# Kernel optimization log

Hardware: AMD Instinct MI355X
Metric: run time of the kernel (lower is better)

Reference implementation:

```python
import jax, jax.numpy as jnp
import numpy as np


def setup_inputs() -> dict:
    key = jax.random.key(0)
    k1, k2 = jax.random.split(key)
    H = W = 4096
    input1 = jax.random.normal(k1, (1, 1, H, W), dtype=jnp.float32)   # moving image
    input2 = jax.random.normal(k2, (1, 2, H, W), dtype=jnp.float32)   # dense flow (dH, dW)
    return {"input1": input1, "input2": input2}


def reference(input1, input2):
    # input1: [B=1, C=1, H, W] image; input2: [B=1, 2, H, W] displacement field
    B, C, H, W = input1.shape
    f32 = jnp.float32

    # identity mesh (matches torch.linspace outer-product construction)
    h_mesh = jnp.broadcast_to(jnp.arange(H, dtype=f32)[None, :, None], (B, H, W))
    w_mesh = jnp.broadcast_to(jnp.arange(W, dtype=f32)[None, None, :], (B, H, W))

    # warped sampling coordinates, shifted by +1 for the zero-padding border
    H_up = (input2[:, 0] + h_mesh).reshape(-1) + 1.0   # [B*H*W]
    W_up = (input2[:, 1] + w_mesh).reshape(-1) + 1.0

    # zero-pad image by 1 pixel on each spatial side
    img = jnp.pad(input1, ((0, 0), (0, 0), (1, 1), (1, 1)))  # [B, C, H+2, W+2]
    Hp, Wp = H + 2, W + 2

    hf = jnp.floor(H_up).astype(jnp.int32)
    hc = hf + 1
    wf = jnp.floor(W_up).astype(jnp.int32)
    wc = wf + 1
    hf = jnp.clip(hf, 0, Hp - 1)
    hc = jnp.clip(hc, 0, Hp - 1)
    wf = jnp.clip(wf, 0, Wp - 1)
    wc = jnp.clip(wc, 0, Wp - 1)

    img_flat = img.reshape(-1)  # B = C = 1
    val_000 = img_flat[hf * Wp + wf]
    val_010 = img_flat[hc * Wp + wf]
    val_001 = img_flat[hf * Wp + wc]
    val_011 = img_flat[hc * Wp + wc]

    dH = hc.astype(f32) - H_up
    dW = wc.astype(f32) - W_up
    out = (val_000 * (dW * dH)
           + val_010 * (dW * (1.0 - dH))
           + val_001 * ((1.0 - dW) * dH)
           + val_011 * ((1.0 - dW) * (1.0 - dH)))

    # [B*H*W] -> [B, H, W, C] -> [B, C, H, W]
    return out.reshape(B, H, W, C).transpose(0, 3, 1, 2)
```

## Files before the change

kernel.cpp:

```cpp
#include <hip/hip_runtime.h>


#define IMG_H 4096
#define IMG_W 4096

typedef float f2  __attribute__((ext_vector_type(2)));
typedef float f2u __attribute__((ext_vector_type(2), aligned(4)));

__global__ __launch_bounds__(256) void warp_bilinear_kernel(
    const float* __restrict__ img,
    const float* __restrict__ flow,
    float* __restrict__ out)
{
    const int HW   = IMG_H * IMG_W;
    const int lane = threadIdx.x & 63;
    const int wv   = threadIdx.x >> 6;
    const int w0   = blockIdx.x * 128 + lane * 2;
    const int h0   = blockIdx.y * 8 + wv * 2;

    int rowidx[2];
    rowidx[0] = h0 * IMG_W + w0;
    rowidx[1] = rowidx[0] + IMG_W;

    f2 fh[2], fw[2];
    #pragma unroll
    for (int r = 0; r < 2; ++r)
        fh[r] = __builtin_nontemporal_load((const f2*)(flow + rowidx[r]));
    #pragma unroll
    for (int r = 0; r < 2; ++r)
        fw[r] = __builtin_nontemporal_load((const f2*)(flow + HW + rowidx[r]));

    int   o0[2][2], o1[2][2];
    float a0x[2][2], a0y[2][2], a1x[2][2], a1y[2][2];

    #pragma unroll
    for (int r = 0; r < 2; ++r) {
        #pragma unroll
        for (int c = 0; c < 2; ++c) {
            const int h = h0 + r;
            const int w = w0 + c;
            float Hu = (fh[r][c] + (float)h) + 1.0f;
            float Wu = (fw[r][c] + (float)w) + 1.0f;

            int hf = (int)floorf(Hu);
            int wf = (int)floorf(Wu);
            int hc = hf + 1;
            int wc = wf + 1;

            int hfc = min(max(hf, 0), IMG_H + 1);
            int hcc = min(max(hc, 0), IMG_H + 1);
            int wfc = min(max(wf, 0), IMG_W + 1);
            int wcc = min(max(wc, 0), IMG_W + 1);

            float dH = (float)hcc - Hu;
            float dW = (float)wcc - Wu;

            int rf = hfc - 1, rc = hcc - 1, cf = wfc - 1, cc = wcc - 1;
            bool rf_in = (unsigned)rf < IMG_H;
            bool rc_in = (unsigned)rc < IMG_H;
            bool cf_in = (unsigned)cf < IMG_W;
            bool cc_in = (unsigned)cc < IMG_W;

            int rf_cl = min(max(rf, 0), IMG_H - 1);
            int rc_cl = min(max(rc, 0), IMG_H - 1);
            int cf_cl = min(max(cf, 0), IMG_W - 1);
            int cc_cl = min(max(cc, 0), IMG_W - 1);
            int cb    = min(max(cf, 0), IMG_W - 2);

            int sf = cf_cl - cb;
            int sc = cc_cl - cb;

            o0[r][c] = (rf_cl << 12) + cb;
            o1[r][c] = (rc_cl << 12) + cb;

            float A = dW * dH;
            float B = dW * (1.0f - dH);
            float C = (1.0f - dW) * dH;
            float D = (1.0f - dW) * (1.0f - dH);
            float w00 = (rf_in && cf_in) ? A : 0.0f;
            float w10 = (rc_in && cf_in) ? B : 0.0f;
            float w01 = (rf_in && cc_in) ? C : 0.0f;
            float w11 = (rc_in && cc_in) ? D : 0.0f;

            a0x[r][c] = (sf ? 0.0f : w00) + (sc ? 0.0f : w01);
            a0y[r][c] = (sf ? w00 : 0.0f) + (sc ? w01 : 0.0f);
            a1x[r][c] = (sf ? 0.0f : w10) + (sc ? 0.0f : w11);
            a1y[r][c] = (sf ? w10 : 0.0f) + (sc ? w11 : 0.0f);
        }
    }

    f2u p0[2][2], p1[2][2];
    #pragma unroll
    for (int r = 0; r < 2; ++r) {
        #pragma unroll
        for (int c = 0; c < 2; ++c) {
            p0[r][c] = *(const f2u*)(img + o0[r][c]);
            p1[r][c] = *(const f2u*)(img + o1[r][c]);
        }
    }

    #pragma unroll
    for (int r = 0; r < 2; ++r) {
        f2 res;
        #pragma unroll
        for (int c = 0; c < 2; ++c) {
            res[c] = p0[r][c].x * a0x[r][c] + p0[r][c].y * a0y[r][c]
                   + p1[r][c].x * a1x[r][c] + p1[r][c].y * a1y[r][c];
        }
        __builtin_nontemporal_store(res, (f2*)(out + rowidx[r]));
    }
}

extern "C" void kernel_launch(void* const* d_in, const int* in_sizes, int n_in,
                              void* d_out, int out_size, void* d_ws, size_t ws_size,
                              hipStream_t stream) {
    const float* img  = (const float*)d_in[0];
    const float* flow = (const float*)d_in[1];
    float* out = (float*)d_out;

    dim3 grid(IMG_W / 128, IMG_H / 8);
    dim3 block(256);
    warp_bilinear_kernel<<<grid, block, 0, stream>>>(img, flow, out);
}
```

Baseline: 243.6 us.

## Stage image tile with halo in shared memory for bilinear gathers

Each block now cooperatively loads a 16x128 image tile plus an 8-pixel halo into LDS using vectorized loads. The bilinear taps are read from shared memory instead of global memory, with a fallback to global loads whenever a tap falls outside the staged window. The block tile also grows so each thread handles four rows instead of two. The goal is to replace scattered global gathers with cheap LDS reads, at the cost of extra halo traffic, a block-wide barrier and more LDS use per block.

```diff
diff --git a/kernel.cpp b/kernel.cpp
--- a/kernel.cpp
+++ b/kernel.cpp
@@ -3,111 +3,165 @@
 
 #define IMG_H 4096
 #define IMG_W 4096
+#define TR 16
+#define TC 128
+#define HALO 8
+#define SR (TR + 2 * HALO)
+#define SC (TC + 2 * HALO)
+#define SC4 (SC / 4)
+#define NCHUNK (SR * SC4)
 
 typedef float f2  __attribute__((ext_vector_type(2)));
 typedef float f2u __attribute__((ext_vector_type(2), aligned(4)));
+typedef float f4  __attribute__((ext_vector_type(4)));
 
 __global__ __launch_bounds__(256) void warp_bilinear_kernel(
     const float* __restrict__ img,
     const float* __restrict__ flow,
     float* __restrict__ out)
 {
+    __shared__ float tile[SR * SC];
+
     const int HW   = IMG_H * IMG_W;
-    const int lane = threadIdx.x & 63;
-    const int wv   = threadIdx.x >> 6;
-    const int w0   = blockIdx.x * 128 + lane * 2;
-    const int h0   = blockIdx.y * 8 + wv * 2;
-
-    int rowidx[2];
-    rowidx[0] = h0 * IMG_W + w0;
-    rowidx[1] = rowidx[0] + IMG_W;
-
-    f2 fh[2], fw[2];
-    #pragma unroll
-    for (int r = 0; r < 2; ++r)
-        fh[r] = __builtin_nontemporal_load((const f2*)(flow + rowidx[r]));
-    #pragma unroll
-    for (int r = 0; r < 2; ++r)
-        fw[r] = __builtin_nontemporal_load((const f2*)(flow + HW + rowidx[r]));
-
-    int   o0[2][2], o1[2][2];
-    float a0x[2][2], a0y[2][2], a1x[2][2], a1y[2][2];
+    const int tid  = threadIdx.x;
+    const int lane = tid & 63;
+    const int wv   = tid >> 6;
+    const int w0   = blockIdx.x * TC + lane * 2;
+    const int h0   = blockIdx.y * TR + wv * 4;
+    const int r_lo = blockIdx.y * TR - HALO;
+    const int c_lo = blockIdx.x * TC - HALO;
 
     #pragma unroll
-    for (int r = 0; r < 2; ++r) {
-        #pragma unroll
-        for (int c = 0; c < 2; ++c) {
-            const int h = h0 + r;
-            const int w = w0 + c;
-            float Hu = (fh[r][c] + (float)h) + 1.0f;
-            float Wu = (fw[r][c] + (float)w) + 1.0f;
-
-            int hf = (int)floorf(Hu);
-            int wf = (int)floorf(Wu);
-            int hc = hf + 1;
-            int wc = wf + 1;
-
-            int hfc = min(max(hf, 0), IMG_H + 1);
-            int hcc = min(max(hc, 0), IMG_H + 1);
-            int wfc = min(max(wf, 0), IMG_W + 1);
-            int wcc = min(max(wc, 0), IMG_W + 1);
-
-            float dH = (float)hcc - Hu;
-            float dW = (float)wcc - Wu;
-
-            int rf = hfc - 1, rc = hcc - 1, cf = wfc - 1, cc = wcc - 1;
-            bool rf_in = (unsigned)rf < IMG_H;
-            bool rc_in = (unsigned)rc < IMG_H;
-            bool cf_in = (unsigned)cf < IMG_W;
-            bool cc_in = (unsigned)cc < IMG_W;
-
-            int rf_cl = min(max(rf, 0), IMG_H - 1);
-            int rc_cl = min(max(rc, 0), IMG_H - 1);
-            int cf_cl = min(max(cf, 0), IMG_W - 1);
-            int cc_cl = min(max(cc, 0), IMG_W - 1);
-            int cb    = min(max(cf, 0), IMG_W - 2);
-
-            int sf = cf_cl - cb;
-            int sc = cc_cl - cb;
-
-            o0[r][c] = (rf_cl << 12) + cb;
-            o1[r][c] = (rc_cl << 12) + cb;
-
-            float A = dW * dH;
-            float B = dW * (1.0f - dH);
-            float C = (1.0f - dW) * dH;
-            float D = (1.0f - dW) * (1.0f - dH);
-            float w00 = (rf_in && cf_in) ? A : 0.0f;
-            float w10 = (rc_in && cf_in) ? B : 0.0f;
-            float w01 = (rf_in && cc_in) ? C : 0.0f;
-            float w11 = (rc_in && cc_in) ? D : 0.0f;
-
-            a0x[r][c] = (sf ? 0.0f : w00) + (sc ? 0.0f : w01);
-            a0y[r][c] = (sf ? w00 : 0.0f) + (sc ? w01 : 0.0f);
-            a1x[r][c] = (sf ? 0.0f : w10) + (sc ? 0.0f : w11);
-            a1y[r][c] = (sf ? w10 : 0.0f) + (sc ? w11 : 0.0f);
+    for (int it = 0; it < 5; ++it) {
+        int t = tid + it * 256;
+        if (t < NCHUNK) {
+            int i  = t / SC4;
+            int m  = t - i * SC4;
+            int gr = min(max(r_lo + i, 0), IMG_H - 1);
+            int gc = min(max(c_lo + 4 * m, 0), IMG_W - 4);
+            f4 v = *(const f4*)(img + gr * IMG_W + gc);
+            *(f4*)(tile + i * SC + 4 * m) = v;
         }
     }
 
-    f2u p0[2][2], p1[2][2];
+    int rowidx[4];
+    f2  fh[4], fw[4];
     #pragma unroll
-    for (int r = 0; r < 2; ++r) {
-        #pragma unroll
-        for (int c = 0; c < 2; ++c) {
-            p0[r][c] = *(const f2u*)(img + o0[r][c]);
-            p1[r][c] = *(const f2u*)(img + o1[r][c]);
-        }
-    }
+    for (int r = 0; r < 4; ++r)
+        rowidx[r] = (h0 + r) * IMG_W + w0;
+    #pragma unroll
+    for (int r = 0; r < 4; ++r)
+        fh[r] = __builtin_nontemporal_load((const f2*)(flow + rowidx[r]));
+    #pragma unroll
+    for (int r = 0; r < 4; ++r)
+        fw[r] = __builtin_nontemporal_load((const f2*)(flow + HW + rowidx[r]));
+
+    __syncthreads();
 
     #pragma unroll
-    for (int r = 0; r < 2; ++r) {
-        f2 res;
+    for (int g = 0; g < 2; ++g) {
+        int   li0[2][2], li1[2][2];
+        int   ob0[2][2], ob1[2][2];
+        float a0x[2][2], a0y[2][2], a1x[2][2], a1y[2][2];
+        bool  ok = true;
+
         #pragma unroll
-        for (int c = 0; c < 2; ++c) {
-            res[c] = p0[r][c].x * a0x[r][c] + p0[r][c].y * a0y[r][c]
-                   + p1[r][c].x * a1x[r][c] + p1[r][c].y * a1y[r][c];
+        for (int rr = 0; rr < 2; ++rr) {
+            const int r = 2 * g + rr;
+            #pragma unroll
+            for (int c = 0; c < 2; ++c) {
+                const int h = h0 + r;
+                const int w = w0 + c;
+                float Hu = (fh[r][c] + (float)h) + 1.0f;
+                float Wu = (fw[r][c] + (float)w) + 1.0f;
+
+                int hf = (int)floorf(Hu);
+                int wf = (int)floorf(Wu);
+                int hc = hf + 1;
+                int wc = wf + 1;
+
+                int hfc = min(max(hf, 0), IMG_H + 1);
+                int hcc = min(max(hc, 0), IMG_H + 1);
+                int wfc = min(max(wf, 0), IMG_W + 1);
+                int wcc = min(max(wc, 0), IMG_W + 1);
+
+                float dH = (float)hcc - Hu;
+                float dW = (float)wcc - Wu;
+
+                int rf = hfc - 1, rc = hcc - 1, cf = wfc - 1, cc = wcc - 1;
+                bool rf_in = (unsigned)rf < IMG_H;
+                bool rc_in = (unsigned)rc < IMG_H;
+                bool cf_in = (unsigned)cf < IMG_W;
+                bool cc_in = (unsigned)cc < IMG_W;
+
+                int rf_cl = min(max(rf, 0), IMG_H - 1);
+                int rc_cl = min(max(rc, 0), IMG_H - 1);
+                int cf_cl = min(max(cf, 0), IMG_W - 1);
+                int cc_cl = min(max(cc, 0), IMG_W - 1);
+                int cb    = min(max(cf, 0), IMG_W - 2);
+
+                int sf = cf_cl - cb;
+                int sc = cc_cl - cb;
+
+                int i0 = rf_cl - r_lo;
+                int i1 = rc_cl - r_lo;
+                int jb = cb - c_lo;
+                ok = ok && ((unsigned)i0 < SR) && ((unsigned)i1 < SR)
+                        && ((unsigned)jb < (SC - 1));
+                li0[rr][c] = i0 * SC + jb;
+                li1[rr][c] = i1 * SC + jb;
+                ob0[rr][c] = (rf_cl << 12) + cb;
+                ob1[rr][c] = (rc_cl << 12) + cb;
+
+                float A = dW * dH;
+                float B = dW * (1.0f - dH);
+                float C = (1.0f - dW) * dH;
+                float D = (1.0f - dW) * (1.0f - dH);
+                float w00 = (rf_in && cf_in) ? A : 0.0f;
+                float w10 = (rc_in && cf_in) ? B : 0.0f;
+                float w01 = (rf_in && cc_in) ? C : 0.0f;
+                float w11 = (rc_in && cc_in) ? D : 0.0f;
+
+                a0x[rr][c] = (sf ? 0.0f : w00) + (sc ? 0.0f : w01);
+                a0y[rr][c] = (sf ? w00 : 0.0f) + (sc ? w01 : 0.0f);
+                a1x[rr][c] = (sf ? 0.0f : w10) + (sc ? 0.0f : w11);
+                a1y[rr][c] = (sf ? w10 : 0.0f) + (sc ? w11 : 0.0f);
+            }
         }
-        __builtin_nontemporal_store(res, (f2*)(out + rowidx[r]));
+
+        float q0x[2][2], q0y[2][2], q1x[2][2], q1y[2][2];
+        if (__builtin_expect(ok, 1)) {
+            #pragma unroll
+            for (int rr = 0; rr < 2; ++rr)
+                #pragma unroll
+                for (int c = 0; c < 2; ++c) {
+                    q0x[rr][c] = tile[li0[rr][c]];
+                    q0y[rr][c] = tile[li0[rr][c] + 1];
+                    q1x[rr][c] = tile[li1[rr][c]];
+                    q1y[rr][c] = tile[li1[rr][c] + 1];
+                }
+        } else {
+            #pragma unroll
+            for (int rr = 0; rr < 2; ++rr)
+                #pragma unroll
+                for (int c = 0; c < 2; ++c) {
+                    f2u p0 = *(const f2u*)(img + ob0[rr][c]);
+                    f2u p1 = *(const f2u*)(img + ob1[rr][c]);
+                    q0x[rr][c] = p0.x; q0y[rr][c] = p0.y;
+                    q1x[rr][c] = p1.x; q1y[rr][c] = p1.y;
+                }
+        }
+
+        #pragma unroll
+        for (int rr = 0; rr < 2; ++rr) {
+            f2 res;
+            #pragma unroll
+            for (int c = 0; c < 2; ++c) {
+                res[c] = q0x[rr][c] * a0x[rr][c] + q0y[rr][c] * a0y[rr][c]
+                       + q1x[rr][c] * a1x[rr][c] + q1y[rr][c] * a1y[rr][c];
+            }
+            __builtin_nontemporal_store(res, (f2*)(out + rowidx[2 * g + rr]));
+        }
     }
 }
 
@@ -118,7 +172,7 @@
     const float* flow = (const float*)d_in[1];
     float* out = (float*)d_out;
 
-    dim3 grid(IMG_W / 128, IMG_H / 8);
+    dim3 grid(IMG_W / TC, IMG_H / TR);
     dim3 block(256);
     warp_bilinear_kernel<<<grid, block, 0, stream>>>(img, flow, out);
 }
```

Measured after the change: 239.1 us. Within noise of the previous version (-1.9%).

## Stage per-wave image tile with halo in LDS for bilinear gathers

Applied to the files above, without the earlier changes.

Each wavefront cooperatively loads a 32x48 image tile, its 16x32 output region plus an 8-pixel halo, into its own LDS slab. The four bilinear taps are then gathered from LDS rather than through scattered global loads. Pixels whose sample falls outside the halo or near the image border fall back to the original global-memory path. The goal is to replace uncoalesced global gathers with one coalesced tile load plus fast LDS reads, at the cost of reading about three times the image area, extra LDS use and a divergent fallback branch.

```diff
diff --git a/kernel.cpp b/kernel.cpp
--- a/kernel.cpp
+++ b/kernel.cpp
@@ -3,111 +3,198 @@
 
 #define IMG_H 4096
 #define IMG_W 4096
+#define HALO 8
+#define WTR 16
+#define WTC 32
+#define SRW (WTR + 2 * HALO)
+#define SCW (WTC + 2 * HALO)
+#define LSTRIDE 52
+#define SLAB (SRW * LSTRIDE)
+#define NCPR (SCW / 4)
 
 typedef float f2  __attribute__((ext_vector_type(2)));
 typedef float f2u __attribute__((ext_vector_type(2), aligned(4)));
-
-__global__ __launch_bounds__(256) void warp_bilinear_kernel(
+typedef float f4  __attribute__((ext_vector_type(4)));
+
+__device__ __forceinline__ float full_pixel(const float* __restrict__ img,
+                                            float fhv, float fwv, int h, int w)
+{
+    float Hu = (fhv + (float)h) + 1.0f;
+    float Wu = (fwv + (float)w) + 1.0f;
+
+    int hf = (int)floorf(Hu);
+    int wf = (int)floorf(Wu);
+    int hc = hf + 1;
+    int wc = wf + 1;
+
+    int hfc = min(max(hf, 0), IMG_H + 1);
+    int hcc = min(max(hc, 0), IMG_H + 1);
+    int wfc = min(max(wf, 0), IMG_W + 1);
+    int wcc = min(max(wc, 0), IMG_W + 1);
+
+    float dH = (float)hcc - Hu;
+    float dW = (float)wcc - Wu;
+
+    int rf = hfc - 1, rc = hcc - 1, cf = wfc - 1, cc = wcc - 1;
+    bool rf_in = (unsigned)rf < IMG_H;
+    bool rc_in = (unsigned)rc < IMG_H;
+    bool cf_in = (unsigned)cf < IMG_W;
+    bool cc_in = (unsigned)cc < IMG_W;
+
+    int rf_cl = min(max(rf, 0), IMG_H - 1);
+    int rc_cl = min(max(rc, 0), IMG_H - 1);
+    int cf_cl = min(max(cf, 0), IMG_W - 1);
+    int cc_cl = min(max(cc, 0), IMG_W - 1);
+    int cb    = min(max(cf, 0), IMG_W - 2);
+
+    int sf = cf_cl - cb;
+    int sc = cc_cl - cb;
+
+    float A = dW * dH;
+    float B = dW * (1.0f - dH);
+    float C = (1.0f - dW) * dH;
+    float D = (1.0f - dW) * (1.0f - dH);
+    float w00 = (rf_in && cf_in) ? A : 0.0f;
+    float w10 = (rc_in && cf_in) ? B : 0.0f;
+    float w01 = (rf_in && cc_in) ? C : 0.0f;
+    float w11 = (rc_in && cc_in) ? D : 0.0f;
+
+    float a0x = (sf ? 0.0f : w00) + (sc ? 0.0f : w01);
+    float a0y = (sf ? w00 : 0.0f) + (sc ? w01 : 0.0f);
+    float a1x = (sf ? 0.0f : w10) + (sc ? 0.0f : w11);
+    float a1y = (sf ? w10 : 0.0f) + (sc ? w11 : 0.0f);
+
+    f2u p0 = *(const f2u*)(img + (rf_cl << 12) + cb);
+    f2u p1 = *(const f2u*)(img + (rc_cl << 12) + cb);
+    return p0.x * a0x + p0.y * a0y + p1.x * a1x + p1.y * a1y;
+}
+
+__global__ __launch_bounds__(256, 6) void warp_bilinear_kernel(
     const float* __restrict__ img,
     const float* __restrict__ flow,
     float* __restrict__ out)
 {
-    const int HW   = IMG_H * IMG_W;
-    const int lane = threadIdx.x & 63;
-    const int wv   = threadIdx.x >> 6;
-    const int w0   = blockIdx.x * 128 + lane * 2;
-    const int h0   = blockIdx.y * 8 + wv * 2;
-
-    int rowidx[2];
-    rowidx[0] = h0 * IMG_W + w0;
-    rowidx[1] = rowidx[0] + IMG_W;
-
-    f2 fh[2], fw[2];
-    #pragma unroll
-    for (int r = 0; r < 2; ++r)
-        fh[r] = __builtin_nontemporal_load((const f2*)(flow + rowidx[r]));
-    #pragma unroll
-    for (int r = 0; r < 2; ++r)
-        fw[r] = __builtin_nontemporal_load((const f2*)(flow + HW + rowidx[r]));
-
-    int   o0[2][2], o1[2][2];
-    float a0x[2][2], a0y[2][2], a1x[2][2], a1y[2][2];
-
-    #pragma unroll
-    for (int r = 0; r < 2; ++r) {
+    __shared__ float lds[4 * SLAB];
+
+    const int HW    = IMG_H * IMG_W;
+    const int tid   = threadIdx.x;
+    const int lane  = tid & 63;
+    const int wid   = tid >> 6;
+    const int cpair = lane & 15;
+    const int rgrp  = lane >> 4;
+    const int bx    = blockIdx.x, by = blockIdx.y;
+
+    float* slab = lds + wid * SLAB;
+
+    const int c0    = bx * 128 + wid * WTC + cpair * 2;
+    const int wr_lo = by * WTR - HALO;
+    const int wc_lo = bx * 128 + wid * WTC - HALO;
+    const int rbase = -1 - wr_lo;
+    const int cbase = -1 - wc_lo;
+
+    f4 S[6];
+    #pragma unroll
+    for (int j = 0; j < 6; ++j) {
+        int ch  = lane + 64 * j;
+        int row = ch / NCPR;
+        int m   = ch - row * NCPR;
+        int gr  = min(max(wr_lo + row, 0), IMG_H - 1);
+        int gc  = min(max(wc_lo + 4 * m, 0), IMG_W - 4);
+        S[j] = *(const f4*)(img + gr * IMG_W + gc);
+    }
+
+    int RI[4]; f2 FH[4], FW[4];
+    #pragma unroll
+    for (int k = 0; k < 4; ++k)
+        RI[k] = (by * WTR + rgrp + 4 * k) * IMG_W + c0;
+    #pragma unroll
+    for (int k = 0; k < 4; ++k)
+        FH[k] = __builtin_nontemporal_load((const f2*)(flow + RI[k]));
+    #pragma unroll
+    for (int k = 0; k < 4; ++k)
+        FW[k] = __builtin_nontemporal_load((const f2*)(flow + HW + RI[k]));
+
+    #pragma unroll
+    for (int j = 0; j < 6; ++j) {
+        int ch  = lane + 64 * j;
+        int row = ch / NCPR;
+        int m   = ch - row * NCPR;
+        *(f4*)(slab + row * LSTRIDE + 4 * m) = S[j];
+    }
+
+    #pragma unroll
+    for (int g = 0; g < 2; ++g) {
+        int   li[2][2];
+        float A_[2][2], B_[2][2], C_[2][2], D_[2][2];
+        bool  ok = true;
+
         #pragma unroll
-        for (int c = 0; c < 2; ++c) {
-            const int h = h0 + r;
-            const int w = w0 + c;
-            float Hu = (fh[r][c] + (float)h) + 1.0f;
-            float Wu = (fw[r][c] + (float)w) + 1.0f;
-
-            int hf = (int)floorf(Hu);
-            int wf = (int)floorf(Wu);
-            int hc = hf + 1;
-            int wc = wf + 1;
-
-            int hfc = min(max(hf, 0), IMG_H + 1);
-            int hcc = min(max(hc, 0), IMG_H + 1);
-            int wfc = min(max(wf, 0), IMG_W + 1);
-            int wcc = min(max(wc, 0), IMG_W + 1);
-
-            float dH = (float)hcc - Hu;
-            float dW = (float)wcc - Wu;
-
-            int rf = hfc - 1, rc = hcc - 1, cf = wfc - 1, cc = wcc - 1;
-            bool rf_in = (unsigned)rf < IMG_H;
-            bool rc_in = (unsigned)rc < IMG_H;
-            bool cf_in = (unsigned)cf < IMG_W;
-            bool cc_in = (unsigned)cc < IMG_W;
-
-            int rf_cl = min(max(rf, 0), IMG_H - 1);
-            int rc_cl = min(max(rc, 0), IMG_H - 1);
-            int cf_cl = min(max(cf, 0), IMG_W - 1);
-            int cc_cl = min(max(cc, 0), IMG_W - 1);
-            int cb    = min(max(cf, 0), IMG_W - 2);
-
-            int sf = cf_cl - cb;
-            int sc = cc_cl - cb;
-
-            o0[r][c] = (rf_cl << 12) + cb;
-            o1[r][c] = (rc_cl << 12) + cb;
-
-            float A = dW * dH;
-            float B = dW * (1.0f - dH);
-            float C = (1.0f - dW) * dH;
-            float D = (1.0f - dW) * (1.0f - dH);
-            float w00 = (rf_in && cf_in) ? A : 0.0f;
-            float w10 = (rc_in && cf_in) ? B : 0.0f;
-            float w01 = (rf_in && cc_in) ? C : 0.0f;
-            float w11 = (rc_in && cc_in) ? D : 0.0f;
-
-            a0x[r][c] = (sf ? 0.0f : w00) + (sc ? 0.0f : w01);
-            a0y[r][c] = (sf ? w00 : 0.0f) + (sc ? w01 : 0.0f);
-            a1x[r][c] = (sf ? 0.0f : w10) + (sc ? 0.0f : w11);
-            a1y[r][c] = (sf ? w10 : 0.0f) + (sc ? w11 : 0.0f);
-        }
-    }
-
-    f2u p0[2][2], p1[2][2];
-    #pragma unroll
-    for (int r = 0; r < 2; ++r) {
+        for (int kk = 0; kk < 2; ++kk) {
+            const int k = 2 * g + kk;
+            const int h = by * WTR + rgrp + 4 * k;
+            #pragma unroll
+            for (int c = 0; c < 2; ++c) {
+                float Hu = (FH[k][c] + (float)h) + 1.0f;
+                float Wu = (FW[k][c] + (float)(c0 + c)) + 1.0f;
+
+                int hf = (int)floorf(Hu);
+                int wf = (int)floorf(Wu);
+                float dH = (float)(hf + 1) - Hu;
+                float dW = (float)(wf + 1) - Wu;
+
+                int i0 = hf + rbase;
+                int jb = wf + cbase;
+
+                ok = ok && ((unsigned)(hf - 1) < IMG_H - 1)
+                        && ((unsigned)(wf - 1) < IMG_W - 1)
+                        && ((unsigned)i0 < SRW - 1)
+                        && ((unsigned)jb < SCW - 1);
+                li[kk][c] = i0 * LSTRIDE + jb;
+
+                float omH = 1.0f - dH, omW = 1.0f - dW;
+                A_[kk][c] = dW * dH;
+                C_[kk][c] = omW * dH;
+                B_[kk][c] = dW * omH;
+                D_[kk][c] = omW * omH;
+            }
+        }
+
+        float res[2][2];
+        if (__builtin_expect(ok, 1)) {
+            float q0x[2][2], q0y[2][2], q1x[2][2], q1y[2][2];
+            #pragma unroll
+            for (int kk = 0; kk < 2; ++kk)
+                #pragma unroll
+                for (int c = 0; c < 2; ++c) {
+                    q0x[kk][c] = slab[li[kk][c]];
+                    q0y[kk][c] = slab[li[kk][c] + 1];
+                    q1x[kk][c] = slab[li[kk][c] + LSTRIDE];
+                    q1y[kk][c] = slab[li[kk][c] + LSTRIDE + 1];
+                }
+            #pragma unroll
+            for (int kk = 0; kk < 2; ++kk)
+                #pragma unroll
+                for (int c = 0; c < 2; ++c)
+                    res[kk][c] = q0x[kk][c] * A_[kk][c] + q0y[kk][c] * C_[kk][c]
+                               + q1x[kk][c] * B_[kk][c] + q1y[kk][c] * D_[kk][c];
+        }
+        if (__builtin_expect(!ok, 0)) {
+            #pragma unroll
+            for (int kk = 0; kk < 2; ++kk) {
+                const int k = 2 * g + kk;
+                const int h = by * WTR + rgrp + 4 * k;
+                #pragma unroll
+                for (int c = 0; c < 2; ++c)
+                    res[kk][c] = full_pixel(img, FH[k][c], FW[k][c],
+                                            h, c0 + c);
+            }
+        }
+
         #pragma unroll
-        for (int c = 0; c < 2; ++c) {
-            p0[r][c] = *(const f2u*)(img + o0[r][c]);
-            p1[r][c] = *(const f2u*)(img + o1[r][c]);
-        }
-    }
-
-    #pragma unroll
-    for (int r = 0; r < 2; ++r) {
-        f2 res;
-        #pragma unroll
-        for (int c = 0; c < 2; ++c) {
-            res[c] = p0[r][c].x * a0x[r][c] + p0[r][c].y * a0y[r][c]
-                   + p1[r][c].x * a1x[r][c] + p1[r][c].y * a1y[r][c];
-        }
-        __builtin_nontemporal_store(res, (f2*)(out + rowidx[r]));
+        for (int kk = 0; kk < 2; ++kk) {
+            f2 v; v[0] = res[kk][0]; v[1] = res[kk][1];
+            __builtin_nontemporal_store(v, (f2*)(out + RI[2 * g + kk]));
+        }
     }
 }
 
@@ -118,7 +205,7 @@
     const float* flow = (const float*)d_in[1];
     float* out = (float*)d_out;
 
-    dim3 grid(IMG_W / 128, IMG_H / 8);
+    dim3 grid(IMG_W / 128, IMG_H / WTR);
     dim3 block(256);
     warp_bilinear_kernel<<<grid, block, 0, stream>>>(img, flow, out);
 }
```

New measurement: 239.1 us. No clear change (-1.8%).
